# Optimization experiments

Measured on AMD Instinct MI355X. Metric: run time of the kernel, lower is better.

The kernel has to match this reference:

```python
import jax, jax.numpy as jnp
import numpy as np

N = 100000      # nodes
E = 1600000     # edges (avg degree 16)
F_IN = 128      # num_features
H = 64          # hidden_dim
C = 7           # num_classes


def setup_inputs() -> dict:
    key = jax.random.key(0)
    ks = jax.random.split(key, 9)
    x = jax.random.normal(ks[0], (N, F_IN), dtype=jnp.float32)
    edge_index = jax.random.randint(ks[1], (2, E), 0, N, dtype=jnp.int32)
    s1 = 1.0 / np.sqrt(F_IN)
    s2 = 1.0 / np.sqrt(H)
    # SAGEConv1: lin_l applied to aggregated neighbors, lin_r to root
    W1l = jax.random.uniform(ks[2], (F_IN, H), jnp.float32, -s1, s1)
    W1r = jax.random.uniform(ks[3], (F_IN, H), jnp.float32, -s1, s1)
    b1 = jax.random.uniform(ks[4], (H,), jnp.float32, -s1, s1)
    # SAGEConv2
    W2l = jax.random.uniform(ks[5], (H, C), jnp.float32, -s2, s2)
    W2r = jax.random.uniform(ks[6], (H, C), jnp.float32, -s2, s2)
    b2 = jax.random.uniform(ks[7], (C,), jnp.float32, -s2, s2)
    return {"x": x, "edge_index": edge_index, "W1l": W1l, "W1r": W1r,
            "b1": b1, "W2l": W2l, "W2r": W2r, "b2": b2}


def _segment_mean(vals, idx, num_segments):
    # scatter-mean: sum messages per destination node, divide by in-degree
    sums = jax.ops.segment_sum(vals, idx, num_segments=num_segments)
    cnt = jax.ops.segment_sum(jnp.ones(idx.shape, vals.dtype), idx,
                              num_segments=num_segments)
    return sums / jnp.maximum(cnt, 1.0)[:, None]


def reference(x, edge_index, W1l, W1r, b1, W2l, W2r, b2):
    src, dst = edge_index[0], edge_index[1]
    # SAGEConv 1: mean of neighbor (src) features at each dst, plus root term
    agg1 = _segment_mean(x[src], dst, N)              # [N, F_IN]
    h = agg1 @ W1l + x @ W1r + b1                     # [N, H]
    h = jax.nn.relu(h)
    # dropout is inactive in eval mode (deterministic reference)
    # SAGEConv 2
    agg2 = _segment_mean(h[src], dst, N)              # [N, H]
    out = agg2 @ W2l + h @ W2r + b2                   # [N, C]
    return jax.nn.log_softmax(out, axis=1)
```

## Files before the change

kernel.cpp:

```cpp
#include <hip/hip_runtime.h>
#include <cstdint>
#include <cstddef>


#define CAP 64
#define BINSZ 128
#define CH 16384

typedef __attribute__((ext_vector_type(8))) short bf16x8v;
typedef __attribute__((ext_vector_type(4))) float f32x4v;

__device__ __forceinline__ float bf2f(unsigned short u) {
  return __uint_as_float(((unsigned int)u) << 16);
}
__device__ __forceinline__ unsigned short f2bf(float f) {
  unsigned int x = __float_as_uint(f);
  unsigned int r = (x + 0x7fffu + ((x >> 16) & 1u)) >> 16;
  return (unsigned short)r;
}

__global__ __launch_bounds__(256) void k_hist(const int* __restrict__ ei,
                                              int* __restrict__ hist,
                                              int E, int NB, int NCH) {
  __shared__ int lcnt[1024];
  const int c = blockIdx.x, t = threadIdx.x;
  for (int i = t; i < NB; i += 256) lcnt[i] = 0;
  __syncthreads();
  const int base = c * CH;
  const int end = min(base + CH, E);
  for (int e = base + t; e < end; e += 256) {
    int d = ei[E + e];
    atomicAdd(&lcnt[d >> 7], 1);
  }
  __syncthreads();
  for (int i = t; i < NB; i += 256) hist[(size_t)i * NCH + c] = lcnt[i];
}

__global__ __launch_bounds__(256) void k_scanA(int* __restrict__ hist,
                                               int* __restrict__ tot,
                                               int NB, int NCH) {
  const int lane = threadIdx.x & 63;
  const int bin = blockIdx.x * 4 + (threadIdx.x >> 6);
  if (bin >= NB) return;
  int* h = hist + (size_t)bin * NCH;
  int carry = 0;
  for (int base = 0; base < NCH; base += 64) {
    int i = base + lane;
    int v = (i < NCH) ? h[i] : 0;
    int incl = v;
    #pragma unroll
    for (int d = 1; d < 64; d <<= 1) {
      int t = __shfl_up(incl, d, 64);
      if (lane >= d) incl += t;
    }
    if (i < NCH) h[i] = carry + incl - v;
    carry += __shfl(incl, 63, 64);
  }
  if (lane == 0) tot[bin] = carry;
}

__global__ __launch_bounds__(64) void k_scanB(const int* __restrict__ tot,
                                              int* __restrict__ binbase, int NB) {
  const int lane = threadIdx.x;
  int carry = 0;
  for (int base = 0; base < NB; base += 64) {
    int i = base + lane;
    int v = (i < NB) ? tot[i] : 0;
    int incl = v;
    #pragma unroll
    for (int d = 1; d < 64; d <<= 1) {
      int t = __shfl_up(incl, d, 64);
      if (lane >= d) incl += t;
    }
    if (i < NB) binbase[i] = carry + incl - v;
    carry += __shfl(incl, 63, 64);
  }
  if (lane == 0) binbase[NB] = carry;
}

__global__ __launch_bounds__(256) void k_scat(const int* __restrict__ ei,
                                              const int* __restrict__ hist,
                                              const int* __restrict__ binbase,
                                              unsigned int* __restrict__ part,
                                              int E, int NB, int NCH) {
  __shared__ int lcur[1024];
  const int c = blockIdx.x, t = threadIdx.x;
  for (int i = t; i < NB; i += 256)
    lcur[i] = hist[(size_t)i * NCH + c] + binbase[i];
  __syncthreads();
  const int base = c * CH;
  const int end = min(base + CH, E);
  for (int e = base + t; e < end; e += 256) {
    int s = ei[e];
    int d = ei[E + e];
    int bin = d >> 7;
    int pos = atomicAdd(&lcur[bin], 1);
    part[pos] = (unsigned)s | ((unsigned)(d & 127) << 17);
  }
}

__global__ __launch_bounds__(256) void k_bucketB(const int* __restrict__ binbase,
                                                 const unsigned int* __restrict__ part,
                                                 int* __restrict__ cnt,
                                                 int* __restrict__ bucket) {
  __shared__ int lbkt[BINSZ * CAP];
  __shared__ int ldeg[BINSZ];
  const int b = blockIdx.x, t = threadIdx.x;
  if (t < BINSZ) ldeg[t] = 0;
  __syncthreads();
  const int e0 = binbase[b], e1 = binbase[b + 1];
  for (int i = e0 + t; i < e1; i += 256) {
    unsigned rec = part[i];
    int loc = rec >> 17;
    int p = atomicAdd(&ldeg[loc], 1);
    if (p < CAP) lbkt[loc * CAP + p] = (int)(rec & 0x1FFFFu);
  }
  __syncthreads();
  if (t < BINSZ) cnt[b * BINSZ + t] = ldeg[t];
  const int4* s4 = (const int4*)lbkt;
  int4* d4 = (int4*)(bucket + (size_t)b * BINSZ * CAP);
  #pragma unroll 2
  for (int i = t; i < BINSZ * CAP / 4; i += 256) d4[i] = s4[i];
}

__global__ __launch_bounds__(256) void k_wprep(const float* __restrict__ W1l,
                                               const float* __restrict__ W1r,
                                               unsigned short* __restrict__ wswz) {
  int idx = blockIdx.x * 256 + threadIdx.x;
  int j = idx & 7;
  int lane = (idx >> 3) & 63;
  int c = (idx >> 9) & 7;
  int t4 = idx >> 12;
  int kk = t4 * 32 + (lane >> 4) * 8 + j;
  int nn = c * 16 + (lane & 15);
  float v = (nn < 64) ? W1l[kk * 64 + nn] : W1r[kk * 64 + (nn - 64)];
  wswz[idx] = f2bf(v);
}

__global__ __launch_bounds__(256) void k_gemm1(
    const float* __restrict__ x,
    const unsigned short* __restrict__ wswz,
    const float* __restrict__ b1,
    unsigned short* __restrict__ xl,
    unsigned short* __restrict__ hroot,
    int Nn) {
  __shared__ unsigned short Bsw[16384];
  const int t = threadIdx.x;
  {
    const uint4* src = (const uint4*)wswz;
    uint4* dst = (uint4*)Bsw;
    #pragma unroll
    for (int i = 0; i < 8; ++i) dst[t + i * 256] = src[t + i * 256];
  }
  __syncthreads();

  const int lane = t & 63;
  const int wid = t >> 6;
  const int quad = lane >> 4;
  const int m = lane & 15;
  const int rowA = blockIdx.x * 64 + wid * 16 + m;
  const float* xrow = x + (size_t)min(rowA, Nn - 1) * 128;

  f32x4v acc[8];
  #pragma unroll
  for (int c = 0; c < 8; ++c) acc[c] = (f32x4v){0.f, 0.f, 0.f, 0.f};

  #pragma unroll
  for (int t4 = 0; t4 < 4; ++t4) {
    const int koff = t4 * 32 + quad * 8;
    float4 a0 = *(const float4*)(xrow + koff);
    float4 a1 = *(const float4*)(xrow + koff + 4);
    bf16x8v af;
    af[0] = (short)f2bf(a0.x); af[1] = (short)f2bf(a0.y);
    af[2] = (short)f2bf(a0.z); af[3] = (short)f2bf(a0.w);
    af[4] = (short)f2bf(a1.x); af[5] = (short)f2bf(a1.y);
    af[6] = (short)f2bf(a1.z); af[7] = (short)f2bf(a1.w);
    #pragma unroll
    for (int c = 0; c < 8; ++c) {
      const bf16x8v bf_ = *(const bf16x8v*)&Bsw[(((t4 * 8 + c) * 64 + lane)) << 3];
      acc[c] = __builtin_amdgcn_mfma_f32_16x16x32_bf16(af, bf_, acc[c], 0, 0, 0);
    }
  }

  const int rbase = blockIdx.x * 64 + wid * 16 + quad * 4;
  #pragma unroll
  for (int c = 0; c < 8; ++c) {
    const int col = c * 16 + m;
    #pragma unroll
    for (int i = 0; i < 4; ++i) {
      const int r = rbase + i;
      if (r < Nn) {
        if (c < 4) xl[(size_t)r * 64 + col] = f2bf(acc[c][i]);
        else       hroot[(size_t)r * 64 + (col - 64)] = f2bf(acc[c][i] + b1[col - 64]);
      }
    }
  }
}

__global__ __launch_bounds__(256) void k_agg1(
    const int* __restrict__ cnt, const int* __restrict__ bucket,
    const unsigned int* __restrict__ xl32, const unsigned int* __restrict__ hroot32,
    unsigned int* __restrict__ hbuf32, int Nn) {
  const int lane = threadIdx.x & 63;
  const int p = lane & 31;
  const int sel = lane >> 5;
  const int gw = blockIdx.x * (blockDim.x >> 6) + (threadIdx.x >> 6);
  const int nw = gridDim.x * (blockDim.x >> 6);
  for (int n = gw; n < Nn; n += nw) {
    int c = cnt[n];
    int m = c < CAP ? c : CAP;
    int sidx = (lane < m) ? bucket[(size_t)n * CAP + lane] : 0;
    if ((unsigned)sidx >= (unsigned)Nn) sidx = 0;
    float accLo = 0.f, accHi = 0.f;
    int i = 0;
    for (; i + 8 <= m; i += 8) {
      int r0 = __shfl(sidx, i + 0 + sel, 64);
      int r1 = __shfl(sidx, i + 2 + sel, 64);
      int r2 = __shfl(sidx, i + 4 + sel, 64);
      int r3 = __shfl(sidx, i + 6 + sel, 64);
      unsigned u0 = xl32[(size_t)r0 * 32 + p];
      unsigned u1 = xl32[(size_t)r1 * 32 + p];
      unsigned u2 = xl32[(size_t)r2 * 32 + p];
      unsigned u3 = xl32[(size_t)r3 * 32 + p];
      accLo += (__uint_as_float(u0 << 16) + __uint_as_float(u1 << 16))
             + (__uint_as_float(u2 << 16) + __uint_as_float(u3 << 16));
      accHi += (__uint_as_float(u0 & 0xFFFF0000u) + __uint_as_float(u1 & 0xFFFF0000u))
             + (__uint_as_float(u2 & 0xFFFF0000u) + __uint_as_float(u3 & 0xFFFF0000u));
    }
    for (; i < m; i += 2) {
      int e = i + sel;
      int esafe = e < m ? e : (m - 1);
      int r = __shfl(sidx, esafe, 64);
      unsigned u = xl32[(size_t)r * 32 + p];
      if (e < m) {
        accLo += __uint_as_float(u << 16);
        accHi += __uint_as_float(u & 0xFFFF0000u);
      }
    }
    accLo += __shfl_xor(accLo, 32, 64);
    accHi += __shfl_xor(accHi, 32, 64);
    if (sel == 0) {
      float dd = c > 0 ? (float)c : 1.f;
      unsigned hu = hroot32[(size_t)n * 32 + p];
      float h0 = fmaxf(accLo / dd + __uint_as_float(hu << 16), 0.f);
      float h1 = fmaxf(accHi / dd + __uint_as_float(hu & 0xFFFF0000u), 0.f);
      hbuf32[(size_t)n * 32 + p] = (unsigned)f2bf(h0) | ((unsigned)f2bf(h1) << 16);
    }
  }
}

__global__ __launch_bounds__(128) void k_gemm2(
    const unsigned short* __restrict__ hbuf,
    const float* __restrict__ W2l, const float* __restrict__ W2r,
    const float* __restrict__ b2,
    float* __restrict__ hl, float* __restrict__ hr, int Nn) {
  __shared__ float tile[128 * 65];
  const int t = threadIdx.x;
  const int rowbase = blockIdx.x * 128;
  for (int idx = t; idx < 128 * 64; idx += 128) {
    int r = idx >> 6, k = idx & 63;
    int n = rowbase + r;
    tile[r * 65 + k] = (n < Nn) ? bf2f(hbuf[(size_t)n * 64 + k]) : 0.f;
  }
  __syncthreads();
  int n = rowbase + t;
  if (n >= Nn) return;
  float al[7] = {0, 0, 0, 0, 0, 0, 0};
  float ar[7] = {0, 0, 0, 0, 0, 0, 0};
  for (int k = 0; k < 64; ++k) {
    float hv = tile[t * 65 + k];
    #pragma unroll
    for (int c = 0; c < 7; ++c) {
      al[c] = fmaf(hv, W2l[k * 7 + c], al[c]);
      ar[c] = fmaf(hv, W2r[k * 7 + c], ar[c]);
    }
  }
  #pragma unroll
  for (int c = 0; c < 7; ++c) {
    hl[(size_t)n * 7 + c] = al[c];
    hr[(size_t)n * 7 + c] = ar[c] + b2[c];
  }
}

__global__ __launch_bounds__(256) void k_out(
    const int* __restrict__ cnt, const int* __restrict__ bucket,
    const float* __restrict__ hl, const float* __restrict__ hr,
    float* __restrict__ out, int Nn) {
  const int lane = threadIdx.x & 63;
  const int c = lane & 7;
  const int sub = lane >> 3;
  const int gw = blockIdx.x * (blockDim.x >> 6) + (threadIdx.x >> 6);
  const int n = gw * 8 + sub;
  if (n >= Nn) return;
  int cn = cnt[n];
  int m = cn < CAP ? cn : CAP;
  const bool act = (c < 7);
  float acc = 0.f;
  for (int e = 0; e < m; ++e) {
    int s = bucket[(size_t)n * CAP + e];
    if ((unsigned)s >= (unsigned)Nn) s = 0;
    if (act) acc += hl[(size_t)s * 7 + c];
  }
  float dd = cn > 0 ? (float)cn : 1.f;
  float v = act ? (acc / dd + hr[(size_t)n * 7 + c]) : -INFINITY;
  float mx = v;
  mx = fmaxf(mx, __shfl_xor(mx, 1, 8));
  mx = fmaxf(mx, __shfl_xor(mx, 2, 8));
  mx = fmaxf(mx, __shfl_xor(mx, 4, 8));
  float ex = act ? expf(v - mx) : 0.f;
  float s2 = ex;
  s2 += __shfl_xor(s2, 1, 8);
  s2 += __shfl_xor(s2, 2, 8);
  s2 += __shfl_xor(s2, 4, 8);
  float res = v - mx - logf(s2);
  if (act) out[(size_t)n * 7 + c] = res;
}

static inline size_t alignup(size_t v) { return (v + 255) & ~(size_t)255; }

extern "C" void kernel_launch(void* const* d_in, const int* in_sizes, int n_in,
                              void* d_out, int out_size, void* d_ws, size_t ws_size,
                              hipStream_t stream) {
  const int N = in_sizes[0] / 128;
  const int E = in_sizes[1] / 2;
  const int NB = (N + BINSZ - 1) / BINSZ;
  const int Np = NB * BINSZ;
  const int NCH = (E + CH - 1) / CH;

  const float* x   = (const float*)d_in[0];
  const int*   ei  = (const int*)d_in[1];
  const float* W1l = (const float*)d_in[2];
  const float* W1r = (const float*)d_in[3];
  const float* b1  = (const float*)d_in[4];
  const float* W2l = (const float*)d_in[5];
  const float* W2r = (const float*)d_in[6];
  const float* b2  = (const float*)d_in[7];
  float* out = (float*)d_out;

  char* p = (char*)d_ws;
  int* hist    = (int*)p;            p += alignup((size_t)NB * NCH * 4);
  int* tot     = (int*)p;            p += alignup((size_t)NB * 4);
  int* binbase = (int*)p;            p += alignup((size_t)(NB + 1) * 4);
  unsigned int* part = (unsigned int*)p; p += alignup((size_t)E * 4);
  int* cnt    = (int*)p;             p += alignup((size_t)Np * 4);
  int* bucket = (int*)p;             p += alignup((size_t)Np * CAP * 4);
  unsigned short* wswz = (unsigned short*)p; p += alignup((size_t)16384 * 2);
  unsigned short* xl    = (unsigned short*)p; p += alignup((size_t)N * 64 * 2);
  unsigned short* hroot = (unsigned short*)p; p += alignup((size_t)N * 64 * 2);
  unsigned short* hbuf  = (unsigned short*)p; p += alignup((size_t)N * 64 * 2);
  float* hl  = (float*)p;            p += alignup((size_t)N * 7 * 4);
  float* hr  = (float*)p;            p += alignup((size_t)N * 7 * 4);

  dim3 b256(256);
  k_hist<<<dim3(NCH), b256, 0, stream>>>(ei, hist, E, NB, NCH);
  k_scanA<<<dim3((NB + 3) / 4), b256, 0, stream>>>(hist, tot, NB, NCH);
  k_scanB<<<dim3(1), dim3(64), 0, stream>>>(tot, binbase, NB);
  k_scat<<<dim3(NCH), b256, 0, stream>>>(ei, hist, binbase, part, E, NB, NCH);
  k_bucketB<<<dim3(NB), b256, 0, stream>>>(binbase, part, cnt, bucket);
  k_wprep<<<dim3(64), b256, 0, stream>>>(W1l, W1r, wswz);
  k_gemm1<<<dim3((N + 63) / 64), b256, 0, stream>>>(x, wswz, b1, xl, hroot, N);
  k_agg1<<<dim3(2048), b256, 0, stream>>>(cnt, bucket,
      (const unsigned int*)xl, (const unsigned int*)hroot, (unsigned int*)hbuf, N);
  k_gemm2<<<dim3((N + 127) / 128), dim3(128), 0, stream>>>(hbuf, W2l, W2r, b2, hl, hr, N);
  const int waves_out = (N + 7) / 8;
  k_out<<<dim3((waves_out + 3) / 4), b256, 0, stream>>>(cnt, bucket, hl, hr, out, N);
}
```

Baseline: 281.3 us.

## Use readlane in agg1, pad hl/hr to stride 8, batch bucket loads in k_out

In k_agg1 the wave now walks all edges of a node together, reading each neighbour index with readlane instead of splitting edges across two half-waves with shuffles. This removes the final cross-half reduction but leaves the upper 32 lanes doing redundant loads. The layer-2 projections hl/hr are padded from stride 7 to 8 floats so each row is aligned. k_out now loads 8 bucket indices in one coalesced read per group and broadcasts them with shuffles, instead of every lane loading each index serially.

```diff
diff --git a/kernel.cpp b/kernel.cpp
--- a/kernel.cpp
+++ b/kernel.cpp
@@ -203,7 +203,6 @@
     unsigned int* __restrict__ hbuf32, int Nn) {
   const int lane = threadIdx.x & 63;
   const int p = lane & 31;
-  const int sel = lane >> 5;
   const int gw = blockIdx.x * (blockDim.x >> 6) + (threadIdx.x >> 6);
   const int nw = gridDim.x * (blockDim.x >> 6);
   for (int n = gw; n < Nn; n += nw) {
@@ -214,32 +213,38 @@
     float accLo = 0.f, accHi = 0.f;
     int i = 0;
     for (; i + 8 <= m; i += 8) {
-      int r0 = __shfl(sidx, i + 0 + sel, 64);
-      int r1 = __shfl(sidx, i + 2 + sel, 64);
-      int r2 = __shfl(sidx, i + 4 + sel, 64);
-      int r3 = __shfl(sidx, i + 6 + sel, 64);
+      int r0 = __builtin_amdgcn_readlane(sidx, i + 0);
+      int r1 = __builtin_amdgcn_readlane(sidx, i + 1);
+      int r2 = __builtin_amdgcn_readlane(sidx, i + 2);
+      int r3 = __builtin_amdgcn_readlane(sidx, i + 3);
+      int r4 = __builtin_amdgcn_readlane(sidx, i + 4);
+      int r5 = __builtin_amdgcn_readlane(sidx, i + 5);
+      int r6 = __builtin_amdgcn_readlane(sidx, i + 6);
+      int r7 = __builtin_amdgcn_readlane(sidx, i + 7);
       unsigned u0 = xl32[(size_t)r0 * 32 + p];
       unsigned u1 = xl32[(size_t)r1 * 32 + p];
       unsigned u2 = xl32[(size_t)r2 * 32 + p];
       unsigned u3 = xl32[(size_t)r3 * 32 + p];
-      accLo += (__uint_as_float(u0 << 16) + __uint_as_float(u1 << 16))
-             + (__uint_as_float(u2 << 16) + __uint_as_float(u3 << 16));
-      accHi += (__uint_as_float(u0 & 0xFFFF0000u) + __uint_as_float(u1 & 0xFFFF0000u))
-             + (__uint_as_float(u2 & 0xFFFF0000u) + __uint_as_float(u3 & 0xFFFF0000u));
-    }
-    for (; i < m; i += 2) {
-      int e = i + sel;
-      int esafe = e < m ? e : (m - 1);
-      int r = __shfl(sidx, esafe, 64);
+      unsigned u4 = xl32[(size_t)r4 * 32 + p];
+      unsigned u5 = xl32[(size_t)r5 * 32 + p];
+      unsigned u6 = xl32[(size_t)r6 * 32 + p];
+      unsigned u7 = xl32[(size_t)r7 * 32 + p];
+      accLo += ((__uint_as_float(u0 << 16) + __uint_as_float(u1 << 16))
+              + (__uint_as_float(u2 << 16) + __uint_as_float(u3 << 16)))
+             + ((__uint_as_float(u4 << 16) + __uint_as_float(u5 << 16))
+              + (__uint_as_float(u6 << 16) + __uint_as_float(u7 << 16)));
+      accHi += ((__uint_as_float(u0 & 0xFFFF0000u) + __uint_as_float(u1 & 0xFFFF0000u))
+              + (__uint_as_float(u2 & 0xFFFF0000u) + __uint_as_float(u3 & 0xFFFF0000u)))
+             + ((__uint_as_float(u4 & 0xFFFF0000u) + __uint_as_float(u5 & 0xFFFF0000u))
+              + (__uint_as_float(u6 & 0xFFFF0000u) + __uint_as_float(u7 & 0xFFFF0000u)));
+    }
+    for (; i < m; ++i) {
+      int r = __builtin_amdgcn_readlane(sidx, i);
       unsigned u = xl32[(size_t)r * 32 + p];
-      if (e < m) {
-        accLo += __uint_as_float(u << 16);
-        accHi += __uint_as_float(u & 0xFFFF0000u);
-      }
-    }
-    accLo += __shfl_xor(accLo, 32, 64);
-    accHi += __shfl_xor(accHi, 32, 64);
-    if (sel == 0) {
+      accLo += __uint_as_float(u << 16);
+      accHi += __uint_as_float(u & 0xFFFF0000u);
+    }
+    if (lane < 32) {
       float dd = c > 0 ? (float)c : 1.f;
       unsigned hu = hroot32[(size_t)n * 32 + p];
       float h0 = fmaxf(accLo / dd + __uint_as_float(hu << 16), 0.f);
@@ -277,9 +282,11 @@
   }
   #pragma unroll
   for (int c = 0; c < 7; ++c) {
-    hl[(size_t)n * 7 + c] = al[c];
-    hr[(size_t)n * 7 + c] = ar[c] + b2[c];
-  }
+    hl[(size_t)n * 8 + c] = al[c];
+    hr[(size_t)n * 8 + c] = ar[c] + b2[c];
+  }
+  hl[(size_t)n * 8 + 7] = 0.f;
+  hr[(size_t)n * 8 + 7] = 0.f;
 }
 
 __global__ __launch_bounds__(256) void k_out(
@@ -296,13 +303,19 @@
   int m = cn < CAP ? cn : CAP;
   const bool act = (c < 7);
   float acc = 0.f;
-  for (int e = 0; e < m; ++e) {
-    int s = bucket[(size_t)n * CAP + e];
-    if ((unsigned)s >= (unsigned)Nn) s = 0;
-    if (act) acc += hl[(size_t)s * 7 + c];
+  for (int e0 = 0; e0 < m; e0 += 8) {
+    int bv = (e0 + c < m) ? bucket[(size_t)n * CAP + e0 + c] : 0;
+    #pragma unroll
+    for (int cc = 0; cc < 8; ++cc) {
+      if (e0 + cc < m) {
+        int s = __shfl(bv, (lane & 56) + cc, 64);
+        if ((unsigned)s >= (unsigned)Nn) s = 0;
+        if (act) acc += hl[(size_t)s * 8 + c];
+      }
+    }
   }
   float dd = cn > 0 ? (float)cn : 1.f;
-  float v = act ? (acc / dd + hr[(size_t)n * 7 + c]) : -INFINITY;
+  float v = act ? (acc / dd + hr[(size_t)n * 8 + c]) : -INFINITY;
   float mx = v;
   mx = fmaxf(mx, __shfl_xor(mx, 1, 8));
   mx = fmaxf(mx, __shfl_xor(mx, 2, 8));
@@ -348,8 +361,8 @@
   unsigned short* xl    = (unsigned short*)p; p += alignup((size_t)N * 64 * 2);
   unsigned short* hroot = (unsigned short*)p; p += alignup((size_t)N * 64 * 2);
   unsigned short* hbuf  = (unsigned short*)p; p += alignup((size_t)N * 64 * 2);
-  float* hl  = (float*)p;            p += alignup((size_t)N * 7 * 4);
-  float* hr  = (float*)p;            p += alignup((size_t)N * 7 * 4);
+  float* hl  = (float*)p;            p += alignup((size_t)N * 8 * 4);
+  float* hr  = (float*)p;            p += alignup((size_t)N * 8 * 4);
 
   dim3 b256(256);
   k_hist<<<dim3(NCH), b256, 0, stream>>>(ei, hist, E, NB, NCH);
```

After: 282.1 us. About the same (+0.3%).
